# Optimization experiments

Measured on AMD Instinct MI355X. Metric: run time of the kernel, lower is better.

The kernel has to match this reference:

```python
import jax, jax.numpy as jnp
import numpy as np

M, K, N = 65536, 512, 512
EPS = 1e-05


def setup_inputs() -> dict:
    key = jax.random.key(0)
    k1, k2, k3 = jax.random.split(key, 3)
    x = jax.random.normal(k1, (M, K), dtype=jnp.float32)
    # int8 weight buffer in [-128, 127]
    weight_int8 = jax.random.randint(k2, (N, K), -128, 128, dtype=jnp.int32).astype(jnp.int8)
    # realistic per-output-channel dequant scales (max-abs / 127 of an fp weight)
    weight_scale = jax.random.uniform(k3, (N,), dtype=jnp.float32, minval=0.001, maxval=0.02)
    return {"x": x, "weight_int8": weight_int8, "weight_scale": weight_scale}


def reference(x, weight_int8, weight_scale):
    # dynamic per-tensor quantization of the activation
    x_scale = jnp.maximum(jnp.max(jnp.abs(x)) / 127.0, EPS)
    x_int8 = jnp.clip(jnp.round(x / x_scale), -128, 127).astype(jnp.int8)
    out_int32 = jnp.matmul(x_int8, weight_int8.T, preferred_element_type=jnp.int32)
    # dequantize: per-tensor input scale * per-row weight scale
    out = out_int32.astype(jnp.float32) * (x_scale * weight_scale[None, :])
    return out
```

## Files before the change

kernel.cpp:

```cpp
#include <hip/hip_runtime.h>


#define M_DIM 65536
#define K_DIM 512
#define N_DIM 512
#define EPSF  1e-5f

typedef int int32x4 __attribute__((ext_vector_type(4)));

#define WS_ABS    0
#define WS_WPACK  32768

__device__ inline unsigned int pack_w4(int4 v) {
    return (v.x & 0xff) | ((v.y & 0xff) << 8) |
           ((v.z & 0xff) << 16) | ((unsigned)v.w << 24);
}

__device__ inline unsigned int quantpack4(float4 f, float inv) {
    const float C = 12582912.0f;
    unsigned int u0 = __float_as_uint(fmaf(f.x, inv, C));
    unsigned int u1 = __float_as_uint(fmaf(f.y, inv, C));
    unsigned int u2 = __float_as_uint(fmaf(f.z, inv, C));
    unsigned int u3 = __float_as_uint(fmaf(f.w, inv, C));
    unsigned int lo = __builtin_amdgcn_perm(u1, u0, 0x0C0C0400u);
    unsigned int hi = __builtin_amdgcn_perm(u3, u2, 0x04000C0Cu);
    return lo | hi;
}

__global__ void absmax1_pack_kernel(const float* __restrict__ x,
                                    const int* __restrict__ wi,
                                    unsigned int* __restrict__ ws_abs,
                                    unsigned int* __restrict__ wp) {
    const int b = blockIdx.x;
    const int t = threadIdx.x;
    if (b < 4096) {
        __shared__ float red[4];
        const float4* x4 = (const float4*)x;
        const int base = b * 2048;
        float m = 0.0f;
        #pragma unroll
        for (int j = 0; j < 8; ++j) {
            float4 v = x4[base + j * 256 + t];
            m = fmaxf(m, fmaxf(fmaxf(fabsf(v.x), fabsf(v.y)),
                               fmaxf(fabsf(v.z), fabsf(v.w))));
        }
        #pragma unroll
        for (int off = 32; off > 0; off >>= 1)
            m = fmaxf(m, __shfl_xor(m, off));
        if ((t & 63) == 0) red[t >> 6] = m;
        __syncthreads();
        if (t == 0) {
            float bm = fmaxf(fmaxf(red[0], red[1]), fmaxf(red[2], red[3]));
            atomicMax(ws_abs, __float_as_uint(bm));
        }
    } else {
        const int bb = b - 4096;
        #pragma unroll
        for (int j = 0; j < 4; ++j) {
            int d = bb * 1024 + j * 256 + t;
            wp[d] = pack_w4(((const int4*)wi)[d]);
        }
    }
}

__global__ __launch_bounds__(256, 2) void quant_gemm_kernel(
    const float* __restrict__ x, const signed char* __restrict__ w,
    const float* __restrict__ wscale, const unsigned int* __restrict__ ws_abs,
    float* __restrict__ out) {
    __shared__ __attribute__((aligned(16))) signed char Lds[64 * 1024];

    const int t    = threadIdx.x;
    const int wave = t >> 6;
    const int lane = t & 63;
    const int quad = lane >> 4;
    const int l16  = lane & 15;
    const int b    = blockIdx.x;
    const int m0   = b * 128;

    const float mx  = __uint_as_float(ws_abs[0]);
    const float s   = fmaxf(mx / 127.0f, EPSF);
    const float inv = 1.0f / s;

    {
        const float4* xs = (const float4*)(x + (size_t)m0 * K_DIM);
        const int rsub = t >> 5;
        const int csub = (t & 31) * 16;
        #pragma unroll
        for (int j = 0; j < 16; ++j) {
            const int fi = j * 1024 + t * 4;
            float4 v0 = xs[fi + 0];
            float4 v1 = xs[fi + 1];
            float4 v2 = xs[fi + 2];
            float4 v3 = xs[fi + 3];
            int32x4 p;
            p.x = (int)quantpack4(v0, inv);
            p.y = (int)quantpack4(v1, inv);
            p.z = (int)quantpack4(v2, inv);
            p.w = (int)quantpack4(v3, inv);
            const int row  = j * 8 + rsub;
            const int addr = (row * 512 + csub) ^ ((row & 7) << 4);
            *(int32x4*)(Lds + addr) = p;
        }
    }
    __syncthreads();

    int32x4 a0[8], a1[8];
    {
        const int r0 = wave * 32 + l16;
        const int r1 = r0 + 16;
        #pragma unroll
        for (int k = 0; k < 8; ++k) {
            const int c = quad * 16 + k * 64;
            a0[k] = *(const int32x4*)(Lds + ((r0 * 512 + c) ^ ((r0 & 7) << 4)));
            a1[k] = *(const int32x4*)(Lds + ((r1 * 512 + c) ^ ((r1 & 7) << 4)));
        }
    }
    __syncthreads();

    const int mw = m0 + wave * 32;

    const int start = ((b ^ (b >> 8)) & 1) * 2;

    {
        const int n0 = ((start) & 3) * 128;
        #pragma unroll
        for (int cc = 0; cc < 2; ++cc) {
            int c = wave * 2 + cc;
            #pragma unroll
            for (int tt = 0; tt < 8; ++tt) {
                const signed char* g = w + (long)(n0 + tt * 16 + l16) * K_DIM
                                         + c * 64 + quad * 16;
                __builtin_amdgcn_global_load_lds(
                    (const __attribute__((address_space(1))) unsigned int*)g,
                    (__attribute__((address_space(3))) unsigned int*)(Lds + (c * 8 + tt) * 1024),
                    16, 0, 0);
            }
        }
    }

    for (int i = 0; i < 4; ++i) {
        const int bx = (start + i) & 3;
        const int n0 = bx * 128;
        __syncthreads();

        int32x4 acc0[8] = {};
        int32x4 acc1[8] = {};
        #pragma unroll
        for (int k = 0; k < 8; ++k) {
            const signed char* bbase = Lds + k * 8192 + lane * 16;
            #pragma unroll
            for (int tt = 0; tt < 8; ++tt) {
                int32x4 bfrag = *(const int32x4*)(bbase + tt * 1024);
                acc0[tt] = __builtin_amdgcn_mfma_i32_16x16x64_i8(a0[k], bfrag, acc0[tt], 0, 0, 0);
                acc1[tt] = __builtin_amdgcn_mfma_i32_16x16x64_i8(a1[k], bfrag, acc1[tt], 0, 0, 0);
            }
        }
        __syncthreads();

        if (i < 3) {
            const int n1 = ((start + i + 1) & 3) * 128;
            #pragma unroll
            for (int cc = 0; cc < 2; ++cc) {
                int c = wave * 2 + cc;
                #pragma unroll
                for (int tt = 0; tt < 8; ++tt) {
                    const signed char* g = w + (long)(n1 + tt * 16 + l16) * K_DIM
                                             + c * 64 + quad * 16;
                    __builtin_amdgcn_global_load_lds(
                        (const __attribute__((address_space(1))) unsigned int*)g,
                        (__attribute__((address_space(3))) unsigned int*)(Lds + (c * 8 + tt) * 1024),
                        16, 0, 0);
                }
            }
        }

        #pragma unroll
        for (int tt = 0; tt < 8; ++tt) {
            int n = n0 + tt * 16 + l16;
            float c = s * wscale[n];
            float* o0 = out + (long)(mw + quad * 4) * N_DIM + n;
            float* o1 = o0 + (long)16 * N_DIM;
            #pragma unroll
            for (int r = 0; r < 4; ++r) {
                o0[(long)r * N_DIM] = (float)acc0[tt][r] * c;
                o1[(long)r * N_DIM] = (float)acc1[tt][r] * c;
            }
        }
    }
}

extern "C" void kernel_launch(void* const* d_in, const int* in_sizes, int n_in,
                              void* d_out, int out_size, void* d_ws, size_t ws_size,
                              hipStream_t stream) {
    const float* x   = (const float*)d_in[0];
    const int*   wi  = (const int*)d_in[1];
    const float* sc  = (const float*)d_in[2];
    float*       out = (float*)d_out;

    unsigned int* ws_abs = (unsigned int*)d_ws;
    unsigned int* wp     = (unsigned int*)((char*)d_ws + WS_WPACK);
    const signed char* w8 = (const signed char*)wp;

    hipMemsetAsync(d_ws, 0, 4, stream);

    absmax1_pack_kernel<<<4160, 256, 0, stream>>>(x, wi, ws_abs, wp);
    quant_gemm_kernel<<<512, 256, 0, stream>>>(x, w8, sc, ws_abs, out);
}
```

Measured before the change: 273.5 us.

## Read weight fragments directly from global memory instead of staging through LDS

Drops the LDS staging of the packed int8 weight tiles (global_load_lds plus barriers and the alternating start order). Each wave now loads its B fragments directly from global memory, relying on L2/L1 caching of the small 256KB weight. This removes the block-wide syncthreads and LDS traffic, but each wave now issues its own redundant global loads and has no explicit prefetch overlap. The LDS is still used only for the A tile. The removed syncthreads after the A-fragment reads is safe because LDS is no longer overwritten.

```diff
diff --git a/kernel.cpp b/kernel.cpp
--- a/kernel.cpp
+++ b/kernel.cpp
@@ -115,62 +115,24 @@
             a1[k] = *(const int32x4*)(Lds + ((r1 * 512 + c) ^ ((r1 & 7) << 4)));
         }
     }
-    __syncthreads();
 
     const int mw = m0 + wave * 32;
 
-    const int start = ((b ^ (b >> 8)) & 1) * 2;
+    const signed char* wb = w + (long)l16 * K_DIM + quad * 16;
 
-    {
-        const int n0 = ((start) & 3) * 128;
-        #pragma unroll
-        for (int cc = 0; cc < 2; ++cc) {
-            int c = wave * 2 + cc;
-            #pragma unroll
-            for (int tt = 0; tt < 8; ++tt) {
-                const signed char* g = w + (long)(n0 + tt * 16 + l16) * K_DIM
-                                         + c * 64 + quad * 16;
-                __builtin_amdgcn_global_load_lds(
-                    (const __attribute__((address_space(1))) unsigned int*)g,
-                    (__attribute__((address_space(3))) unsigned int*)(Lds + (c * 8 + tt) * 1024),
-                    16, 0, 0);
-            }
-        }
-    }
-
-    for (int i = 0; i < 4; ++i) {
-        const int bx = (start + i) & 3;
+    for (int bx = 0; bx < 4; ++bx) {
         const int n0 = bx * 128;
-        __syncthreads();
+        const signed char* wt = wb + (long)n0 * K_DIM;
 
         int32x4 acc0[8] = {};
         int32x4 acc1[8] = {};
         #pragma unroll
         for (int k = 0; k < 8; ++k) {
-            const signed char* bbase = Lds + k * 8192 + lane * 16;
             #pragma unroll
             for (int tt = 0; tt < 8; ++tt) {
-                int32x4 bfrag = *(const int32x4*)(bbase + tt * 1024);
+                int32x4 bfrag = *(const int32x4*)(wt + (long)tt * 16 * K_DIM + k * 64);
                 acc0[tt] = __builtin_amdgcn_mfma_i32_16x16x64_i8(a0[k], bfrag, acc0[tt], 0, 0, 0);
                 acc1[tt] = __builtin_amdgcn_mfma_i32_16x16x64_i8(a1[k], bfrag, acc1[tt], 0, 0, 0);
-            }
-        }
-        __syncthreads();
-
-        if (i < 3) {
-            const int n1 = ((start + i + 1) & 3) * 128;
-            #pragma unroll
-            for (int cc = 0; cc < 2; ++cc) {
-                int c = wave * 2 + cc;
-                #pragma unroll
-                for (int tt = 0; tt < 8; ++tt) {
-                    const signed char* g = w + (long)(n1 + tt * 16 + l16) * K_DIM
-                                             + c * 64 + quad * 16;
-                    __builtin_amdgcn_global_load_lds(
-                        (const __attribute__((address_space(1))) unsigned int*)g,
-                        (__attribute__((address_space(3))) unsigned int*)(Lds + (c * 8 + tt) * 1024),
-                        16, 0, 0);
-                }
             }
         }
 
```

Measured after the change: 304.1 us. 11.2% more time.
